# Kernel tuning notes

Measured on AMD Instinct MI355X. Metric: run time of the kernel, lower is better.

## Reference

```python
import jax, jax.numpy as jnp
import numpy as np

DIM = 512
HEADS = 16
HEAD_DIM = DIM // HEADS
WH, WW = 7, 7
N = WH * WW
OUP = 512
SCALE = HEAD_DIM ** -0.5
NW = 64  # windows per image (mask leading dim)


def _relative_position_index():
    coords = np.stack(np.meshgrid(np.arange(WH), np.arange(WW), indexing='ij'))  # (2,Wh,Ww)
    flat = coords.reshape(2, -1)                           # (2, N)
    rel = flat[:, :, None] - flat[:, None, :]              # (2, N, N)
    rel = rel.transpose(1, 2, 0).astype(np.int64)          # (N, N, 2)
    rel[:, :, 0] += WH - 1
    rel[:, :, 1] += WW - 1
    rel[:, :, 0] *= 2 * WW - 1
    return jnp.asarray(rel.sum(-1))                        # (N, N) int

REL_IDX = _relative_position_index()


def setup_inputs() -> dict:
    key = jax.random.key(0)
    ks = jax.random.split(key, 8)
    B_ = 4096
    x = jax.random.normal(ks[0], (B_, N, DIM), dtype=jnp.float32)
    mask = jnp.zeros((NW, N, N), dtype=jnp.float32)
    qkv_w = jax.random.normal(ks[1], (3 * DIM, DIM), dtype=jnp.float32) * (DIM ** -0.5)
    qkv_b = jax.random.normal(ks[2], (3 * DIM,), dtype=jnp.float32) * 0.02
    table = jax.random.normal(ks[3], ((2 * WH - 1) * (2 * WW - 1), HEADS), dtype=jnp.float32) * 0.02
    proj_w = jax.random.normal(ks[4], (OUP, DIM), dtype=jnp.float32) * (DIM ** -0.5)
    proj_b = jax.random.normal(ks[5], (OUP,), dtype=jnp.float32) * 0.02
    return {"x": x, "mask": mask, "qkv_w": qkv_w, "qkv_b": qkv_b,
            "table": table, "proj_w": proj_w, "proj_b": proj_b}


def reference(x, mask, qkv_w, qkv_b, table, proj_w, proj_b):
    B_, n, c = x.shape
    qkv = x @ qkv_w.T + qkv_b                               # (B_, N, 3C)
    qkv = qkv.reshape(B_, n, 3, HEADS, HEAD_DIM).transpose(2, 0, 3, 1, 4)
    q, k, v = qkv[0], qkv[1], qkv[2]                        # (B_, H, N, hd)
    q = q * SCALE
    attn = jnp.einsum('bhnd,bhmd->bhnm', q, k)              # (B_, H, N, N)
    bias = table[REL_IDX]                                   # (N, N, H) gather
    attn = attn + bias.transpose(2, 0, 1)[None]             # add rel-pos bias
    nW = mask.shape[0]
    attn = attn.reshape(B_ // nW, nW, HEADS, n, n) + mask[None, :, None]
    attn = attn.reshape(B_, HEADS, n, n)
    attn = jax.nn.softmax(attn, axis=-1)
    out = jnp.einsum('bhnm,bhmd->bhnd', attn, v)            # (B_, H, N, hd)
    out = out.transpose(0, 2, 1, 3).reshape(B_, n, c)
    return out @ proj_w.T + proj_b
```

## Files before the change

kernel.cpp:

```cpp
#include <hip/hip_runtime.h>
#include <hip/hip_bf16.h>
#include <stdint.h>

#define DIMC 512
#define HEADS 16
#define HEAD_DIM 32
#define NTOK 49
#define SCALE 0.17677669529663687f

typedef unsigned short u16;
typedef short bf16x8 __attribute__((ext_vector_type(8)));
typedef float f32x4 __attribute__((ext_vector_type(4)));
typedef u16 u16x4 __attribute__((ext_vector_type(4)));
typedef u16 u16x8 __attribute__((ext_vector_type(8)));

#define MFMA16(a, b, c) __builtin_amdgcn_mfma_f32_16x16x32_bf16((a), (b), (c), 0, 0, 0)

__device__ __forceinline__ u16 f2bf(float f) {
  __hip_bfloat16 h = __float2bfloat16(f);
  u16 u;
  __builtin_memcpy(&u, &h, 2);
  return u;
}

__device__ __forceinline__ float bf2f(u16 u) {
  const uint32_t b = ((uint32_t)u) << 16;
  float f;
  __builtin_memcpy(&f, &b, 4);
  return f;
}

__device__ __forceinline__ void gld16(const void* g, void* l) {
  __builtin_amdgcn_global_load_lds(
      (const __attribute__((address_space(1))) uint32_t*)g,
      (__attribute__((address_space(3))) uint32_t*)l, 16, 0, 0);
}

__global__ void cvt_f32_bf16(const float* __restrict__ in, u16* __restrict__ out, int n) {
  const int stride = gridDim.x * blockDim.x;
  for (int i = blockIdx.x * blockDim.x + threadIdx.x; i * 8 < n; i += stride) {
    const float4 v0 = ((const float4*)(in + i * 8))[0];
    const float4 v1 = ((const float4*)(in + i * 8))[1];
    u16x8 r;
    r[0] = f2bf(v0.x); r[1] = f2bf(v0.y); r[2] = f2bf(v0.z); r[3] = f2bf(v0.w);
    r[4] = f2bf(v1.x); r[5] = f2bf(v1.y); r[6] = f2bf(v1.z); r[7] = f2bf(v1.w);
    *(u16x8*)(out + i * 8) = r;
  }
}

__global__ void biasmask_kernel(const float* __restrict__ table, const float* __restrict__ mask,
                                u16* __restrict__ bm) {
  const int wm = blockIdx.x >> 4;
  const int h  = blockIdx.x & 15;
  for (int e = threadIdx.x; e < 4096; e += 256) {
    const int r = e & 3, lane = (e >> 2) & 63, fj = (e >> 8) & 3, fi = e >> 10;
    const int row = fi * 16 + (lane >> 4) * 4 + r;
    const int col = fj * 16 + (lane & 15);
    float v;
    if (row < NTOK && col < NTOK) {
      const int yi = row / 7, xi = row % 7, yj = col / 7, xj = col % 7;
      const int idx = (yi - yj + 6) * 13 + (xi - xj + 6);
      v = table[idx * HEADS + h] + mask[wm * (NTOK * NTOK) + row * NTOK + col];
    } else {
      v = -1e30f;
    }
    bm[(size_t)blockIdx.x * 4096 + e] = f2bf(v);
  }
}

template<bool OUT_BF16, bool QKV_SCALE>
__global__ void gemm_bf16(const u16* __restrict__ Ap, const u16* __restrict__ Bp,
                          const float* __restrict__ bias, void* __restrict__ Cp,
                          int M, int N, int K, int nxt) {
  __shared__ u16 As[128 * 64];
  __shared__ u16 Bs[128 * 64];
  const int t = threadIdx.x;
  const int lane = t & 63;
  const int q = gridDim.x >> 3;
  const int lin = blockIdx.x;
  const int l = (lin & 7) * q + (lin >> 3);
  const int bm0 = (l / nxt) * 128;
  const int bn0 = (l % nxt) * 128;
  const int wv = t >> 6, wr = wv >> 1, wc = wv & 1;
  const int lr = lane & 15, lg = lane >> 4;

  f32x4 acc[4][4] = {};

  int soff[4];
#pragma unroll
  for (int k = 0; k < 4; ++k) {
    const int c = t + 256 * k;
    const int row = c >> 3, sub = c & 7;
    soff[k] = ((sub ^ (row & 7)) * 8);
  }

  const int nK = K >> 6;
  for (int kt = 0; kt < nK; ++kt) {
    const int k0 = kt << 6;
    __syncthreads();
#pragma unroll
    for (int k = 0; k < 4; ++k) {
      const int c = t + 256 * k;
      const int row = c >> 3;
      gld16(Ap + (size_t)(bm0 + row) * K + k0 + soff[k], As + c * 8);
      gld16(Bp + (size_t)(bn0 + row) * K + k0 + soff[k], Bs + c * 8);
    }
    __syncthreads();

#pragma unroll
    for (int kk = 0; kk < 2; ++kk) {
      bf16x8 af[4], bfr[4];
#pragma unroll
      for (int i = 0; i < 4; ++i) {
        const int row = wr * 64 + i * 16 + lr;
        af[i] = *(const bf16x8*)&As[row * 64 + (((kk * 4 + lg) ^ (row & 7)) << 3)];
      }
#pragma unroll
      for (int j = 0; j < 4; ++j) {
        const int row = wc * 64 + j * 16 + lr;
        bfr[j] = *(const bf16x8*)&Bs[row * 64 + (((kk * 4 + lg) ^ (row & 7)) << 3)];
      }
#pragma unroll
      for (int i = 0; i < 4; ++i)
#pragma unroll
        for (int j = 0; j < 4; ++j)
          acc[i][j] = MFMA16(af[i], bfr[j], acc[i][j]);
    }
  }

#pragma unroll
  for (int j = 0; j < 4; ++j) {
    const int col = bn0 + wc * 64 + j * 16 + lr;
    const float bv = bias[col];
    const float sc = (QKV_SCALE && col < DIMC) ? SCALE : 1.0f;
#pragma unroll
    for (int i = 0; i < 4; ++i) {
      const int row0 = bm0 + wr * 64 + i * 16 + lg * 4;
#pragma unroll
      for (int r = 0; r < 4; ++r) {
        const float val = (acc[i][j][r] + bv) * sc;
        if (OUT_BF16)
          ((u16*)Cp)[(size_t)(row0 + r) * N + col] = f2bf(val);
        else
          ((float*)Cp)[(size_t)(row0 + r) * N + col] = val;
      }
    }
  }
}

__global__ void attn_win(const u16* __restrict__ qkv, const u16* __restrict__ bmfrag,
                         u16* __restrict__ aout) {
  __shared__ u16 P[4][64 * 64];
  const int t = threadIdx.x, lane = t & 63, wv = t >> 6;
  const int lr = lane & 15, lg = lane >> 4;
  const int w = blockIdx.x >> 2;
  const int h = ((blockIdx.x & 3) << 2) + wv;
  const size_t base = (size_t)w * NTOK * 1536 + h * HEAD_DIM;

  const u16* bmp = bmfrag + (((size_t)(w & 63) * 16 + h) << 12);
  f32x4 s[4][4];
#pragma unroll
  for (int i = 0; i < 4; ++i)
#pragma unroll
    for (int j = 0; j < 4; ++j) {
      const u16x4 b4 = *(const u16x4*)&bmp[((i * 4 + j) * 64 + lane) * 4];
#pragma unroll
      for (int r = 0; r < 4; ++r) s[i][j][r] = bf2f(b4[r]);
    }

  const bf16x8 zf = {};
  bf16x8 qf[4], kf[4];
#pragma unroll
  for (int i = 0; i < 4; ++i) {
    const int row = i * 16 + lr;
    const size_t roff = base + (size_t)row * 1536 + lg * 8;
    qf[i] = (row < NTOK) ? *(const bf16x8*)&qkv[roff] : zf;
    kf[i] = (row < NTOK) ? *(const bf16x8*)&qkv[roff + DIMC] : zf;
  }

  __builtin_amdgcn_s_setprio(1);
#pragma unroll
  for (int i = 0; i < 4; ++i)
#pragma unroll
    for (int j = 0; j < 4; ++j)
      s[i][j] = MFMA16(qf[i], kf[j], s[i][j]);
  __builtin_amdgcn_s_setprio(0);

  bf16x8 vf[2][2];
#pragma unroll
  for (int ks = 0; ks < 2; ++ks)
#pragma unroll
    for (int dn = 0; dn < 2; ++dn)
#pragma unroll
      for (int e = 0; e < 8; ++e) {
        int kk = ks * 32 + lg * 8 + e;
        kk = kk < NTOK ? kk : 0;
        vf[ks][dn][e] = (short)qkv[base + 2 * DIMC + (size_t)kk * 1536 + dn * 16 + lr];
      }

  u16* Pw = &P[wv][0];
#pragma unroll
  for (int i = 0; i < 4; ++i)
#pragma unroll
    for (int r = 0; r < 4; ++r) {
      const int ii = i * 16 + lg * 4 + r;
#pragma unroll
      for (int j = 0; j < 4; ++j) {
        const int jj = j * 16 + lr;
        Pw[ii * 64 + (((jj >> 3) ^ (ii & 7)) << 3) + (jj & 7)] = f2bf(__expf(s[i][j][r]));
      }
    }

  bf16x8 ones;
#pragma unroll
  for (int e = 0; e < 8; ++e) ones[e] = (short)0x3F80;
  f32x4 o[4][2] = {};
  f32x4 osum[4] = {};
#pragma unroll
  for (int ks = 0; ks < 2; ++ks) {
    __builtin_amdgcn_s_setprio(1);
#pragma unroll
    for (int i = 0; i < 4; ++i) {
      const int row = i * 16 + lr;
      const bf16x8 pa = *(const bf16x8*)&Pw[row * 64 + (((ks * 4 + lg) ^ (row & 7)) << 3)];
#pragma unroll
      for (int dn = 0; dn < 2; ++dn)
        o[i][dn] = MFMA16(pa, vf[ks][dn], o[i][dn]);
      osum[i] = MFMA16(pa, ones, osum[i]);
    }
    __builtin_amdgcn_s_setprio(0);
  }

#pragma unroll
  for (int i = 0; i < 4; ++i)
#pragma unroll
    for (int r = 0; r < 4; ++r) {
      const int row = i * 16 + lg * 4 + r;
      if (row < NTOK) {
        const float rinv = __builtin_amdgcn_rcpf(osum[i][r]);
        const size_t ob = ((size_t)w * NTOK + row) * DIMC + h * HEAD_DIM;
#pragma unroll
        for (int dn = 0; dn < 2; ++dn)
          aout[ob + dn * 16 + lr] = f2bf(o[i][dn][r] * rinv);
      }
    }
}

extern "C" void kernel_launch(void* const* d_in, const int* in_sizes, int n_in,
                              void* d_out, int out_size, void* d_ws, size_t ws_size,
                              hipStream_t stream) {
  const float* x      = (const float*)d_in[0];
  const float* mask   = (const float*)d_in[1];
  const float* qkv_w  = (const float*)d_in[2];
  const float* qkv_b  = (const float*)d_in[3];
  const float* table  = (const float*)d_in[4];
  const float* proj_w = (const float*)d_in[5];
  const float* proj_b = (const float*)d_in[6];
  float* out = (float*)d_out;

  const int M = 4096 * NTOK;

  char* ws = (char*)d_ws;
  u16*   qkv_bf   = (u16*)ws;
  u16*   wqkv_bf  = (u16*)(ws + 616562688ull);
  u16*   wproj_bf = (u16*)(ws + 618135552ull);
  u16*   biasmask = (u16*)(ws + 618659840ull);
  u16*   x_bf     = (u16*)(ws + 627048448ull);
  u16*   attn_bf  = x_bf;

  cvt_f32_bf16<<<768, 256, 0, stream>>>(qkv_w, wqkv_bf, 1536 * 512);
  cvt_f32_bf16<<<256, 256, 0, stream>>>(proj_w, wproj_bf, 512 * 512);
  biasmask_kernel<<<1024, 256, 0, stream>>>(table, mask, biasmask);
  cvt_f32_bf16<<<1792, 256, 0, stream>>>(x, x_bf, M * DIMC);

  gemm_bf16<true, true><<<1568 * 12, 256, 0, stream>>>(
      x_bf, wqkv_bf, qkv_b, qkv_bf, M, 1536, 512, 12);

  attn_win<<<4096 * 4, 256, 0, stream>>>(qkv_bf, biasmask, attn_bf);

  gemm_bf16<false, false><<<1568 * 4, 256, 0, stream>>>(
      attn_bf, wproj_bf, proj_b, out, M, 512, 512, 4);
}
```

Before: 983.8 us.

## Fuse fp32-to-bf16 conversion of x into QKV GEMM and use exp2 softmax

Removes the standalone conversion pass over x. The QKV GEMM now loads fp32 tiles of x directly into LDS and converts them to bf16 when building MFMA fragments. This saves one full read and write of a ~400MB bf16 intermediate, at the cost of doubled LDS for A and the fp32 A tile being re-read from global once per each of the 12 N-tiles (12 column blocks). Separately, the log2(e) factor is folded into the q scale and the bias/mask table so the softmax can use hardware exp2 instead of expf.

```diff
diff --git a/kernel.cpp b/kernel.cpp
--- a/kernel.cpp
+++ b/kernel.cpp
@@ -7,6 +7,7 @@
 #define HEAD_DIM 32
 #define NTOK 49
 #define SCALE 0.17677669529663687f
+#define LOG2E 1.4426950408889634f
 
 typedef unsigned short u16;
 typedef short bf16x8 __attribute__((ext_vector_type(8)));
@@ -60,7 +61,7 @@
     if (row < NTOK && col < NTOK) {
       const int yi = row / 7, xi = row % 7, yj = col / 7, xj = col % 7;
       const int idx = (yi - yj + 6) * 13 + (xi - xj + 6);
-      v = table[idx * HEADS + h] + mask[wm * (NTOK * NTOK) + row * NTOK + col];
+      v = (table[idx * HEADS + h] + mask[wm * (NTOK * NTOK) + row * NTOK + col]) * LOG2E;
     } else {
       v = -1e30f;
     }
@@ -68,12 +69,12 @@
   }
 }
 
-template<bool OUT_BF16, bool QKV_SCALE>
-__global__ void gemm_bf16(const u16* __restrict__ Ap, const u16* __restrict__ Bp,
+template<bool A_F32, bool OUT_BF16, bool QKV_SCALE>
+__global__ void gemm_bf16(const void* __restrict__ Ap, const u16* __restrict__ Bp,
                           const float* __restrict__ bias, void* __restrict__ Cp,
                           int M, int N, int K, int nxt) {
-  __shared__ u16 As[128 * 64];
-  __shared__ u16 Bs[128 * 64];
+  __shared__ u16 As[A_F32 ? 16384 : 8192];
+  __shared__ u16 Bs[8192];
   const int t = threadIdx.x;
   const int lane = t & 63;
   const int q = gridDim.x >> 3;
@@ -86,14 +87,6 @@
 
   f32x4 acc[4][4] = {};
 
-  int soff[4];
-#pragma unroll
-  for (int k = 0; k < 4; ++k) {
-    const int c = t + 256 * k;
-    const int row = c >> 3, sub = c & 7;
-    soff[k] = ((sub ^ (row & 7)) * 8);
-  }
-
   const int nK = K >> 6;
   for (int kt = 0; kt < nK; ++kt) {
     const int k0 = kt << 6;
@@ -102,8 +95,26 @@
     for (int k = 0; k < 4; ++k) {
       const int c = t + 256 * k;
       const int row = c >> 3;
-      gld16(Ap + (size_t)(bm0 + row) * K + k0 + soff[k], As + c * 8);
-      gld16(Bp + (size_t)(bn0 + row) * K + k0 + soff[k], Bs + c * 8);
+      const int sc = ((c & 7) ^ (row & 7)) * 8;
+      gld16(Bp + (size_t)(bn0 + row) * K + k0 + sc, Bs + c * 8);
+    }
+    if (A_F32) {
+      const float* Af = (const float*)Ap;
+#pragma unroll
+      for (int k = 0; k < 8; ++k) {
+        const int c = t + 256 * k;
+        const int row = c >> 4;
+        const int sc = ((c & 15) ^ (row & 15)) * 4;
+        gld16(Af + (size_t)(bm0 + row) * K + k0 + sc, As + c * 8);
+      }
+    } else {
+#pragma unroll
+      for (int k = 0; k < 4; ++k) {
+        const int c = t + 256 * k;
+        const int row = c >> 3;
+        const int sc = ((c & 7) ^ (row & 7)) * 8;
+        gld16((const u16*)Ap + (size_t)(bm0 + row) * K + k0 + sc, As + c * 8);
+      }
     }
     __syncthreads();
 
@@ -113,7 +124,18 @@
 #pragma unroll
       for (int i = 0; i < 4; ++i) {
         const int row = wr * 64 + i * 16 + lr;
-        af[i] = *(const bf16x8*)&As[row * 64 + (((kk * 4 + lg) ^ (row & 7)) << 3)];
+        if (A_F32) {
+          const float* Asf = (const float*)As;
+          const int c0 = kk * 8 + lg * 2;
+          const f32x4 lo = *(const f32x4*)&Asf[row * 64 + (((c0)     ^ (row & 15)) << 2)];
+          const f32x4 hi = *(const f32x4*)&Asf[row * 64 + (((c0 + 1) ^ (row & 15)) << 2)];
+          bf16x8 a;
+          a[0] = f2bf(lo[0]); a[1] = f2bf(lo[1]); a[2] = f2bf(lo[2]); a[3] = f2bf(lo[3]);
+          a[4] = f2bf(hi[0]); a[5] = f2bf(hi[1]); a[6] = f2bf(hi[2]); a[7] = f2bf(hi[3]);
+          af[i] = a;
+        } else {
+          af[i] = *(const bf16x8*)&As[row * 64 + (((kk * 4 + lg) ^ (row & 7)) << 3)];
+        }
       }
 #pragma unroll
       for (int j = 0; j < 4; ++j) {
@@ -132,7 +154,7 @@
   for (int j = 0; j < 4; ++j) {
     const int col = bn0 + wc * 64 + j * 16 + lr;
     const float bv = bias[col];
-    const float sc = (QKV_SCALE && col < DIMC) ? SCALE : 1.0f;
+    const float sc = (QKV_SCALE && col < DIMC) ? SCALE * LOG2E : 1.0f;
 #pragma unroll
     for (int i = 0; i < 4; ++i) {
       const int row0 = bm0 + wr * 64 + i * 16 + lg * 4;
@@ -207,7 +229,8 @@
 #pragma unroll
       for (int j = 0; j < 4; ++j) {
         const int jj = j * 16 + lr;
-        Pw[ii * 64 + (((jj >> 3) ^ (ii & 7)) << 3) + (jj & 7)] = f2bf(__expf(s[i][j][r]));
+        Pw[ii * 64 + (((jj >> 3) ^ (ii & 7)) << 3) + (jj & 7)] =
+            f2bf(__builtin_amdgcn_exp2f(s[i][j][r]));
       }
     }
 
@@ -265,19 +288,17 @@
   u16*   wqkv_bf  = (u16*)(ws + 616562688ull);
   u16*   wproj_bf = (u16*)(ws + 618135552ull);
   u16*   biasmask = (u16*)(ws + 618659840ull);
-  u16*   x_bf     = (u16*)(ws + 627048448ull);
-  u16*   attn_bf  = x_bf;
+  u16*   attn_bf  = (u16*)(ws + 627048448ull);
 
   cvt_f32_bf16<<<768, 256, 0, stream>>>(qkv_w, wqkv_bf, 1536 * 512);
   cvt_f32_bf16<<<256, 256, 0, stream>>>(proj_w, wproj_bf, 512 * 512);
   biasmask_kernel<<<1024, 256, 0, stream>>>(table, mask, biasmask);
-  cvt_f32_bf16<<<1792, 256, 0, stream>>>(x, x_bf, M * DIMC);
-
-  gemm_bf16<true, true><<<1568 * 12, 256, 0, stream>>>(
-      x_bf, wqkv_bf, qkv_b, qkv_bf, M, 1536, 512, 12);
+
+  gemm_bf16<true, true, true><<<1568 * 12, 256, 0, stream>>>(
+      x, wqkv_bf, qkv_b, qkv_bf, M, 1536, 512, 12);
 
   attn_win<<<4096 * 4, 256, 0, stream>>>(qkv_bf, biasmask, attn_bf);
 
-  gemm_bf16<false, false><<<1568 * 4, 256, 0, stream>>>(
+  gemm_bf16<false, false, false><<<1568 * 4, 256, 0, stream>>>(
       attn_bf, wproj_bf, proj_b, out, M, 512, 512, 4);
 }
```

After: 1.174 ms. +19.3%, slower.
